# Optimization experiments

Measured on AMD Instinct MI355X. Metric: run time of the kernel, lower is better.

## Reference

```python
import jax, jax.numpy as jnp
import numpy as np

IN_FEATURES = 4096
OUT_FEATURES = 768
N_BITS = 8
BATCH = 4096


def setup_inputs() -> dict:
    key = jax.random.key(0)
    k1, k2, k3 = jax.random.split(key, 3)
    latent = jax.random.uniform(k1, (BATCH, IN_FEATURES), dtype=jnp.float32)
    true_sum = jax.random.uniform(k2, (BATCH, OUT_FEATURES * N_BITS), dtype=jnp.float32)
    # kaiming-normal-ish init: std = sqrt(2 / fan_in)
    weight = jax.random.normal(k3, (IN_FEATURES, OUT_FEATURES * N_BITS), dtype=jnp.float32) * np.sqrt(2.0 / IN_FEATURES)
    return {"latent": latent, "true_sum": true_sum, "weight": weight, "n_bits": N_BITS}


def reference(latent, true_sum, weight, n_bits):
    in_features = weight.shape[0]
    batch = latent.shape[0]
    # powers of two, MSB negated (two's-complement style decode)
    powers = (2.0 ** jnp.arange(n_bits, dtype=jnp.float32))
    powers = powers.at[-1].multiply(-1.0)

    prob_weights = jax.nn.sigmoid(weight)                      # [in, out*n_bits]
    # decode soft bits -> integer-valued weights: [in, out]
    int_weights = (prob_weights.reshape(in_features, -1, n_bits) * powers).sum(-1)
    # decode target bits -> integer-valued sums: [batch, out]
    int_sum = (true_sum.reshape(batch, -1, n_bits) * powers).sum(-1)

    # (latent.unsqueeze(-1) * int_weights).sum(-2) is exactly a GEMM
    pred = latent @ int_weights                                # [batch, out]

    scale_factor = 2.0 ** (n_bits - 1)
    recon_loss = jnp.mean((pred - int_sum) ** 2) / scale_factor
    polarize_loss = jnp.mean(prob_weights * (1.0 - prob_weights))
    return (recon_loss, polarize_loss)
```

## Files before the change

kernel.cpp:

```cpp
#include <hip/hip_runtime.h>
#include <stdint.h>

#define IN_F   4096
#define OUT_F  768
#define NB     8
#define BATCH  4096
#define WCOLS  (OUT_F*NB)

typedef short  bf16x8  __attribute__((ext_vector_type(8)));
typedef float  f32x4   __attribute__((ext_vector_type(4)));
typedef unsigned short ushort8 __attribute__((ext_vector_type(8)));

__device__ __forceinline__ unsigned short f2bf(float f){
    union { float f; uint32_t u; } v; v.f = f;
    uint32_t u = v.u;
    u += 0x7FFFu + ((u >> 16) & 1u);
    return (unsigned short)(u >> 16);
}

__device__ __forceinline__ void gload16(const void* g, void* l){
    __builtin_amdgcn_global_load_lds(
        (const __attribute__((address_space(1))) unsigned int*)g,
        (__attribute__((address_space(3))) unsigned int*)l, 16, 0, 0);
}

__global__ void prep_latent(const float* __restrict__ lat,
                            unsigned short* __restrict__ abf,
                            float* __restrict__ acc){
    if (blockIdx.x == 0 && threadIdx.x < 4) acc[threadIdx.x] = 0.f;
    int idx = (blockIdx.x * 256 + threadIdx.x) * 8;
    const float4* p = (const float4*)(lat + idx);
    float4 a = p[0], b = p[1];
    ushort8 o;
    o[0]=f2bf(a.x); o[1]=f2bf(a.y); o[2]=f2bf(a.z); o[3]=f2bf(a.w);
    o[4]=f2bf(b.x); o[5]=f2bf(b.y); o[6]=f2bf(b.z); o[7]=f2bf(b.w);
    *(ushort8*)(abf + idx) = o;
}

__global__ void decode_weight(const float* __restrict__ w,
                              unsigned short* __restrict__ bt,
                              float* __restrict__ acc){
    __shared__ unsigned short tile[64][70];
    __shared__ float part[4];
    const int tid = threadIdx.x;
    const int k0 = blockIdx.x * 64;
    const int n0 = blockIdx.y * 64;
    const int j     = tid & 63;
    const int ibase = (tid >> 6) * 16;
    float pol = 0.f;
    #pragma unroll 4
    for (int r = 0; r < 16; ++r){
        int i = ibase + r;
        const float4* src = (const float4*)(w + (size_t)(k0+i)*WCOLS + (size_t)(n0+j)*8);
        float4 a = src[0], b = src[1];
        float x[8] = {a.x,a.y,a.z,a.w,b.x,b.y,b.z,b.w};
        float p[8];
        #pragma unroll
        for (int q = 0; q < 8; ++q){
            p[q] = 1.f / (1.f + __expf(-x[q]));
            pol += p[q] * (1.f - p[q]);
        }
        float iw = p[0] + 2.f*p[1] + 4.f*p[2] + 8.f*p[3]
                 + 16.f*p[4] + 32.f*p[5] + 64.f*p[6] - 128.f*p[7];
        tile[j][i] = f2bf(iw);
    }
    #pragma unroll
    for (int off = 32; off; off >>= 1) pol += __shfl_down(pol, off);
    if ((tid & 63) == 0) part[tid >> 6] = pol;
    __syncthreads();
    const int nrow = tid >> 4;
    const int kb   = (tid & 15) * 4;
    #pragma unroll
    for (int q = 0; q < 4; ++q){
        int n = nrow + q*16;
        uint2 v;
        v.x = *(const unsigned int*)&tile[n][kb];
        v.y = *(const unsigned int*)&tile[n][kb+2];
        *(uint2*)(bt + (size_t)(n0+n)*IN_F + k0 + kb) = v;
    }
    if (tid == 0) atomicAdd(&acc[1], part[0]+part[1]+part[2]+part[3]);
}

#define BM 128
#define BN 96
#define BK 64
#define NT (IN_F/BK)
#define ABYTES (BM*BK*2)
#define BBYTES (BN*BK*2)

__launch_bounds__(256)
__global__ void gemm_loss(const unsigned short* __restrict__ abf,
                          const unsigned short* __restrict__ bt,
                          const float* __restrict__ ts,
                          float* __restrict__ acc){
    __shared__ unsigned short As[2][BM*BK];
    __shared__ unsigned short Bs[2][BN*BK];
    __shared__ float part[4];
    const int tid = threadIdx.x;
    const int w   = tid >> 6;
    const int l   = tid & 63;
    const int s   = l & 15, g = l >> 4;
    const int wr  = w >> 1, wc = w & 1;
    const int m0  = blockIdx.x * BM;
    const int n0  = blockIdx.y * BN;

    f32x4 accv[4][3];
    #pragma unroll
    for (int m = 0; m < 4; ++m)
        #pragma unroll
        for (int n = 0; n < 3; ++n)
            accv[m][n] = (f32x4){0.f,0.f,0.f,0.f};

    const int c8  = tid & 7;
    const int r0  = tid >> 3;
    const int scw = ((c8 ^ (r0 & 7)) << 3);
    const unsigned short* aS = abf + (size_t)(m0 + r0) * IN_F + scw;
    const unsigned short* bS = bt  + (size_t)(n0 + r0) * IN_F + scw;
    char* AsB = (char*)As;
    char* BsB = (char*)Bs;

    #define STAGE(kt, b) do {                                              \
        const int _ko = (kt) * BK;                                         \
        char* _ad = AsB + (b)*ABYTES + tid*16;                             \
        char* _bd = BsB + (b)*BBYTES + tid*16;                             \
        _Pragma("unroll")                                                  \
        for (int _i = 0; _i < 4; ++_i)                                     \
            gload16(aS + (size_t)_i*32*IN_F + _ko, _ad + _i*4096);         \
        _Pragma("unroll")                                                  \
        for (int _i = 0; _i < 3; ++_i)                                     \
            gload16(bS + (size_t)_i*32*IN_F + _ko, _bd + _i*4096);         \
    } while (0)

    #define COMPUTE(b) do {                                                \
        char* _Ab = AsB + (b)*ABYTES;                                      \
        char* _Bb = BsB + (b)*BBYTES;                                      \
        _Pragma("unroll")                                                  \
        for (int _kk = 0; _kk < 2; ++_kk){                                 \
            bf16x8 _af[4], _bf[3];                                         \
            _Pragma("unroll")                                              \
            for (int _m = 0; _m < 4; ++_m){                                \
                int _r  = wr*64 + _m*16 + s;                               \
                int _ch = _r*8 + ((_kk*4 + g) ^ (_r & 7));                 \
                _af[_m] = *(const bf16x8*)(_Ab + _ch*16);                  \
            }                                                              \
            _Pragma("unroll")                                              \
            for (int _n = 0; _n < 3; ++_n){                                \
                int _r  = wc*48 + _n*16 + s;                               \
                int _ch = _r*8 + ((_kk*4 + g) ^ (_r & 7));                 \
                _bf[_n] = *(const bf16x8*)(_Bb + _ch*16);                  \
            }                                                              \
            _Pragma("unroll")                                              \
            for (int _m = 0; _m < 4; ++_m)                                 \
                _Pragma("unroll")                                          \
                for (int _n = 0; _n < 3; ++_n)                             \
                    accv[_m][_n] = __builtin_amdgcn_mfma_f32_16x16x32_bf16(\
                        _af[_m], _bf[_n], accv[_m][_n], 0, 0, 0);          \
        }                                                                  \
    } while (0)

    STAGE(0, 0);
    __syncthreads();
    int cur = 0;
    for (int kt = 0; kt < NT; ++kt){
        if (kt + 1 < NT) STAGE(kt + 1, cur ^ 1);
        COMPUTE(cur);
        __syncthreads();
        cur ^= 1;
    }

    float local = 0.f;
    #pragma unroll
    for (int m = 0; m < 4; ++m){
        int rbase = m0 + wr*64 + m*16 + g*4;
        #pragma unroll
        for (int n = 0; n < 3; ++n){
            int col = n0 + wc*48 + n*16 + s;
            const float* tsp = ts + (size_t)rbase*WCOLS + (size_t)col*8;
            #pragma unroll
            for (int jj = 0; jj < 4; ++jj){
                const float4* q = (const float4*)(tsp + (size_t)jj*WCOLS);
                float4 x = q[0], y = q[1];
                float isum = x.x + 2.f*x.y + 4.f*x.z + 8.f*x.w
                           + 16.f*y.x + 32.f*y.y + 64.f*y.z - 128.f*y.w;
                float d = accv[m][n][jj] - isum;
                local += d*d;
            }
        }
    }
    #pragma unroll
    for (int off = 32; off; off >>= 1) local += __shfl_down(local, off);
    if (l == 0) part[w] = local;
    __syncthreads();
    if (tid == 0){
        atomicAdd(&acc[0], part[0]+part[1]+part[2]+part[3]);
    }
}

__global__ void finalize(const float* __restrict__ acc, float* __restrict__ out){
    out[0] = acc[0] * (1.0f / ((float)BATCH * (float)OUT_F * 128.0f));
    out[1] = acc[1] * (1.0f / ((float)IN_F * (float)WCOLS));
}

extern "C" void kernel_launch(void* const* d_in, const int* in_sizes, int n_in,
                              void* d_out, int out_size, void* d_ws, size_t ws_size,
                              hipStream_t stream){
    const float* latent   = (const float*)d_in[0];
    const float* true_sum = (const float*)d_in[1];
    const float* weight   = (const float*)d_in[2];
    float* acc = (float*)d_ws;
    unsigned short* abf = (unsigned short*)((char*)d_ws + 1024);
    unsigned short* bt  = (unsigned short*)((char*)d_ws + 1024 + (size_t)BATCH*IN_F*2);
    float* out = (float*)d_out;

    prep_latent<<<(BATCH*IN_F)/(256*8), 256, 0, stream>>>(latent, abf, acc);
    decode_weight<<<dim3(IN_F/64, OUT_F/64), 256, 0, stream>>>(weight, bt, acc);
    gemm_loss<<<dim3(BATCH/BM, OUT_F/BN), 256, 0, stream>>>(abf, bt, true_sum, acc);
    finalize<<<1, 1, 0, stream>>>(acc, out);
}
```

Baseline: 125.1 us.

## Use 4-stage LDS pipeline with vmcnt waits and pre-decode true_sum

Replaces the double-buffered GEMM loop with a four-buffer pipeline. Loads run three tiles ahead, and explicit vmcnt waits plus a single barrier per iteration replace the post-compute syncthreads. A separate kernel decodes true_sum into bf16 integer sums, so the GEMM epilogue reads a compact array instead of eight floats per output. The extra LDS cuts occupancy, and the bf16 rounding of the target sums adds precision loss to the loss value.

```diff
diff --git a/kernel.cpp b/kernel.cpp
--- a/kernel.cpp
+++ b/kernel.cpp
@@ -18,11 +18,21 @@
     return (unsigned short)(u >> 16);
 }
 
+__device__ __forceinline__ float bf2f(unsigned short u){
+    union { uint32_t q; float f; } v; v.q = ((uint32_t)u) << 16;
+    return v.f;
+}
+
 __device__ __forceinline__ void gload16(const void* g, void* l){
     __builtin_amdgcn_global_load_lds(
         (const __attribute__((address_space(1))) unsigned int*)g,
         (__attribute__((address_space(3))) unsigned int*)l, 16, 0, 0);
 }
+
+#define WAITV(n) do {                                                   \
+    asm volatile("s_waitcnt vmcnt(" #n ")" ::: "memory");               \
+    __builtin_amdgcn_sched_barrier(0);                                  \
+} while (0)
 
 __global__ void prep_latent(const float* __restrict__ lat,
                             unsigned short* __restrict__ abf,
@@ -81,20 +91,34 @@
     if (tid == 0) atomicAdd(&acc[1], part[0]+part[1]+part[2]+part[3]);
 }
 
+__global__ void ts_decode(const float* __restrict__ ts,
+                          unsigned short* __restrict__ isum){
+    const int tid = threadIdx.x;
+    #pragma unroll
+    for (int k = 0; k < 6; ++k){
+        int e = blockIdx.x * 1536 + k * 256 + tid;
+        const float4* q = (const float4*)(ts + (size_t)e * 8);
+        float4 x = q[0], y = q[1];
+        float v = x.x + 2.f*x.y + 4.f*x.z + 8.f*x.w
+                + 16.f*y.x + 32.f*y.y + 64.f*y.z - 128.f*y.w;
+        isum[e] = f2bf(v);
+    }
+}
+
 #define BM 128
 #define BN 96
 #define BK 64
 #define NT (IN_F/BK)
 #define ABYTES (BM*BK*2)
 #define BBYTES (BN*BK*2)
+#define BUFB   (ABYTES+BBYTES)
 
 __launch_bounds__(256)
 __global__ void gemm_loss(const unsigned short* __restrict__ abf,
                           const unsigned short* __restrict__ bt,
-                          const float* __restrict__ ts,
+                          const unsigned short* __restrict__ isum,
                           float* __restrict__ acc){
-    __shared__ unsigned short As[2][BM*BK];
-    __shared__ unsigned short Bs[2][BN*BK];
+    __shared__ char smem[4*BUFB];
     __shared__ float part[4];
     const int tid = threadIdx.x;
     const int w   = tid >> 6;
@@ -116,13 +140,11 @@
     const int scw = ((c8 ^ (r0 & 7)) << 3);
     const unsigned short* aS = abf + (size_t)(m0 + r0) * IN_F + scw;
     const unsigned short* bS = bt  + (size_t)(n0 + r0) * IN_F + scw;
-    char* AsB = (char*)As;
-    char* BsB = (char*)Bs;
-
-    #define STAGE(kt, b) do {                                              \
+
+    #define STAGE(kt, base) do {                                           \
         const int _ko = (kt) * BK;                                         \
-        char* _ad = AsB + (b)*ABYTES + tid*16;                             \
-        char* _bd = BsB + (b)*BBYTES + tid*16;                             \
+        char* _ad = (base) + tid*16;                                       \
+        char* _bd = (base) + ABYTES + tid*16;                              \
         _Pragma("unroll")                                                  \
         for (int _i = 0; _i < 4; ++_i)                                     \
             gload16(aS + (size_t)_i*32*IN_F + _ko, _ad + _i*4096);         \
@@ -131,9 +153,9 @@
             gload16(bS + (size_t)_i*32*IN_F + _ko, _bd + _i*4096);         \
     } while (0)
 
-    #define COMPUTE(b) do {                                                \
-        char* _Ab = AsB + (b)*ABYTES;                                      \
-        char* _Bb = BsB + (b)*BBYTES;                                      \
+    #define COMPUTE(base) do {                                             \
+        char* _Ab = (base);                                                \
+        char* _Bb = (base) + ABYTES;                                       \
         _Pragma("unroll")                                                  \
         for (int _kk = 0; _kk < 2; ++_kk){                                 \
             bf16x8 _af[4], _bf[3];                                         \
@@ -158,15 +180,24 @@
         }                                                                  \
     } while (0)
 
-    STAGE(0, 0);
-    __syncthreads();
-    int cur = 0;
-    for (int kt = 0; kt < NT; ++kt){
-        if (kt + 1 < NT) STAGE(kt + 1, cur ^ 1);
-        COMPUTE(cur);
-        __syncthreads();
-        cur ^= 1;
-    }
+    char* b0 = smem;
+    char* b1 = smem + BUFB;
+    char* b2 = smem + 2*BUFB;
+    char* b3 = smem + 3*BUFB;
+
+    STAGE(0, b0);
+    STAGE(1, b1);
+    STAGE(2, b2);
+    for (int t = 0; t < NT-3; ++t){
+        WAITV(14);
+        __builtin_amdgcn_s_barrier();
+        STAGE(t+3, b3);
+        COMPUTE(b0);
+        char* tmp = b0; b0 = b1; b1 = b2; b2 = b3; b3 = tmp;
+    }
+    WAITV(14); __builtin_amdgcn_s_barrier(); COMPUTE(b0);
+    WAITV(7);  __builtin_amdgcn_s_barrier(); COMPUTE(b1);
+    WAITV(0);  __builtin_amdgcn_s_barrier(); COMPUTE(b2);
 
     float local = 0.f;
     #pragma unroll
@@ -175,14 +206,10 @@
         #pragma unroll
         for (int n = 0; n < 3; ++n){
             int col = n0 + wc*48 + n*16 + s;
-            const float* tsp = ts + (size_t)rbase*WCOLS + (size_t)col*8;
             #pragma unroll
             for (int jj = 0; jj < 4; ++jj){
-                const float4* q = (const float4*)(tsp + (size_t)jj*WCOLS);
-                float4 x = q[0], y = q[1];
-                float isum = x.x + 2.f*x.y + 4.f*x.z + 8.f*x.w
-                           + 16.f*y.x + 32.f*y.y + 64.f*y.z - 128.f*y.w;
-                float d = accv[m][n][jj] - isum;
+                float is = bf2f(isum[(size_t)(rbase+jj)*OUT_F + col]);
+                float d = accv[m][n][jj] - is;
                 local += d*d;
             }
         }
@@ -208,12 +235,15 @@
     const float* true_sum = (const float*)d_in[1];
     const float* weight   = (const float*)d_in[2];
     float* acc = (float*)d_ws;
-    unsigned short* abf = (unsigned short*)((char*)d_ws + 1024);
-    unsigned short* bt  = (unsigned short*)((char*)d_ws + 1024 + (size_t)BATCH*IN_F*2);
+    unsigned short* abf  = (unsigned short*)((char*)d_ws + 1024);
+    unsigned short* bt   = (unsigned short*)((char*)d_ws + 1024 + (size_t)BATCH*IN_F*2);
+    unsigned short* isum = (unsigned short*)((char*)d_ws + 1024 + (size_t)BATCH*IN_F*2
+                                             + (size_t)OUT_F*IN_F*2);
     float* out = (float*)d_out;
 
     prep_latent<<<(BATCH*IN_F)/(256*8), 256, 0, stream>>>(latent, abf, acc);
     decode_weight<<<dim3(IN_F/64, OUT_F/64), 256, 0, stream>>>(weight, bt, acc);
-    gemm_loss<<<dim3(BATCH/BM, OUT_F/BN), 256, 0, stream>>>(abf, bt, true_sum, acc);
+    ts_decode<<<(BATCH*OUT_F)/(256*6), 256, 0, stream>>>(true_sum, isum);
+    gemm_loss<<<dim3(BATCH/BM, OUT_F/BN), 256, 0, stream>>>(abf, bt, isum, acc);
     finalize<<<1, 1, 0, stream>>>(acc, out);
 }
```

Measured after the change: 133.1 us. 6.4% more time.

## Split-K GEMM into two halves, move loss to separate pass, merge decode kernels

Applied to the files above, without the earlier changes.

The GEMM now uses a split-K of two. It launches 512 blocks instead of 256 so more CUs on the device are occupied, and each block writes its partial prediction slab to workspace. A new loss_pass kernel sums the two slabs, decodes true_sum and reduces the squared error into per-block partials. The latent and weight decode kernels are merged into one launch, and atomics are replaced by deterministic partial buffers that a 256-thread finalize kernel reduces. MFMA sections get s_setprio, in exchange for extra traffic writing and re-reading about 25MB of fp32 prediction slabs.

```diff
diff --git a/kernel.cpp b/kernel.cpp
--- a/kernel.cpp
+++ b/kernel.cpp
@@ -6,6 +6,7 @@
 #define NB     8
 #define BATCH  4096
 #define WCOLS  (OUT_F*NB)
+#define PREDN  (BATCH*OUT_F)
 
 typedef short  bf16x8  __attribute__((ext_vector_type(8)));
 typedef float  f32x4   __attribute__((ext_vector_type(4)));
@@ -24,85 +25,88 @@
         (__attribute__((address_space(3))) unsigned int*)l, 16, 0, 0);
 }
 
-__global__ void prep_latent(const float* __restrict__ lat,
-                            unsigned short* __restrict__ abf,
-                            float* __restrict__ acc){
-    if (blockIdx.x == 0 && threadIdx.x < 4) acc[threadIdx.x] = 0.f;
-    int idx = (blockIdx.x * 256 + threadIdx.x) * 8;
-    const float4* p = (const float4*)(lat + idx);
-    float4 a = p[0], b = p[1];
-    ushort8 o;
-    o[0]=f2bf(a.x); o[1]=f2bf(a.y); o[2]=f2bf(a.z); o[3]=f2bf(a.w);
-    o[4]=f2bf(b.x); o[5]=f2bf(b.y); o[6]=f2bf(b.z); o[7]=f2bf(b.w);
-    *(ushort8*)(abf + idx) = o;
-}
-
-__global__ void decode_weight(const float* __restrict__ w,
-                              unsigned short* __restrict__ bt,
-                              float* __restrict__ acc){
+__launch_bounds__(256)
+__global__ void decode_all(const float* __restrict__ w,
+                           const float* __restrict__ lat,
+                           unsigned short* __restrict__ bt,
+                           unsigned short* __restrict__ abf,
+                           float* __restrict__ polp){
     __shared__ unsigned short tile[64][70];
     __shared__ float part[4];
     const int tid = threadIdx.x;
-    const int k0 = blockIdx.x * 64;
-    const int n0 = blockIdx.y * 64;
-    const int j     = tid & 63;
-    const int ibase = (tid >> 6) * 16;
-    float pol = 0.f;
-    #pragma unroll 4
-    for (int r = 0; r < 16; ++r){
-        int i = ibase + r;
-        const float4* src = (const float4*)(w + (size_t)(k0+i)*WCOLS + (size_t)(n0+j)*8);
-        float4 a = src[0], b = src[1];
-        float x[8] = {a.x,a.y,a.z,a.w,b.x,b.y,b.z,b.w};
-        float p[8];
-        #pragma unroll
-        for (int q = 0; q < 8; ++q){
-            p[q] = 1.f / (1.f + __expf(-x[q]));
-            pol += p[q] * (1.f - p[q]);
+    const int bid = blockIdx.x;
+    if (bid < 768){
+        const int k0 = (bid & 63) * 64;
+        const int n0 = (bid >> 6) * 64;
+        const int j     = tid & 63;
+        const int ibase = (tid >> 6) * 16;
+        float pol = 0.f;
+        #pragma unroll 4
+        for (int r = 0; r < 16; ++r){
+            int i = ibase + r;
+            const float4* src = (const float4*)(w + (size_t)(k0+i)*WCOLS + (size_t)(n0+j)*8);
+            float4 a = src[0], b = src[1];
+            float x[8] = {a.x,a.y,a.z,a.w,b.x,b.y,b.z,b.w};
+            float p[8];
+            #pragma unroll
+            for (int q = 0; q < 8; ++q){
+                p[q] = 1.f / (1.f + __expf(-x[q]));
+                pol += p[q] * (1.f - p[q]);
+            }
+            float iw = p[0] + 2.f*p[1] + 4.f*p[2] + 8.f*p[3]
+                     + 16.f*p[4] + 32.f*p[5] + 64.f*p[6] - 128.f*p[7];
+            tile[j][i] = f2bf(iw);
         }
-        float iw = p[0] + 2.f*p[1] + 4.f*p[2] + 8.f*p[3]
-                 + 16.f*p[4] + 32.f*p[5] + 64.f*p[6] - 128.f*p[7];
-        tile[j][i] = f2bf(iw);
-    }
-    #pragma unroll
-    for (int off = 32; off; off >>= 1) pol += __shfl_down(pol, off);
-    if ((tid & 63) == 0) part[tid >> 6] = pol;
-    __syncthreads();
-    const int nrow = tid >> 4;
-    const int kb   = (tid & 15) * 4;
-    #pragma unroll
-    for (int q = 0; q < 4; ++q){
-        int n = nrow + q*16;
-        uint2 v;
-        v.x = *(const unsigned int*)&tile[n][kb];
-        v.y = *(const unsigned int*)&tile[n][kb+2];
-        *(uint2*)(bt + (size_t)(n0+n)*IN_F + k0 + kb) = v;
-    }
-    if (tid == 0) atomicAdd(&acc[1], part[0]+part[1]+part[2]+part[3]);
+        #pragma unroll
+        for (int off = 32; off; off >>= 1) pol += __shfl_down(pol, off);
+        if ((tid & 63) == 0) part[tid >> 6] = pol;
+        __syncthreads();
+        const int nrow = tid >> 4;
+        const int kb   = (tid & 15) * 4;
+        #pragma unroll
+        for (int q = 0; q < 4; ++q){
+            int n = nrow + q*16;
+            uint2 v;
+            v.x = *(const unsigned int*)&tile[n][kb];
+            v.y = *(const unsigned int*)&tile[n][kb+2];
+            *(uint2*)(bt + (size_t)(n0+n)*IN_F + k0 + kb) = v;
+        }
+        if (tid == 0) polp[bid] = part[0]+part[1]+part[2]+part[3];
+    } else {
+        int idx = ((bid - 768) * 256 + tid) * 8;
+        const float4* p = (const float4*)(lat + idx);
+        float4 a = p[0], b = p[1];
+        ushort8 o;
+        o[0]=f2bf(a.x); o[1]=f2bf(a.y); o[2]=f2bf(a.z); o[3]=f2bf(a.w);
+        o[4]=f2bf(b.x); o[5]=f2bf(b.y); o[6]=f2bf(b.z); o[7]=f2bf(b.w);
+        *(ushort8*)(abf + idx) = o;
+    }
 }
 
 #define BM 128
 #define BN 96
 #define BK 64
-#define NT (IN_F/BK)
+#define NTH 32
 #define ABYTES (BM*BK*2)
 #define BBYTES (BN*BK*2)
-
-__launch_bounds__(256)
-__global__ void gemm_loss(const unsigned short* __restrict__ abf,
+#define BUFB   (ABYTES+BBYTES)
+
+__launch_bounds__(256)
+__global__ void gemm_pred(const unsigned short* __restrict__ abf,
                           const unsigned short* __restrict__ bt,
-                          const float* __restrict__ ts,
-                          float* __restrict__ acc){
-    __shared__ unsigned short As[2][BM*BK];
-    __shared__ unsigned short Bs[2][BN*BK];
-    __shared__ float part[4];
+                          float* __restrict__ pred){
+    __shared__ __align__(16) char smem[2*BUFB];
     const int tid = threadIdx.x;
     const int w   = tid >> 6;
     const int l   = tid & 63;
     const int s   = l & 15, g = l >> 4;
     const int wr  = w >> 1, wc = w & 1;
-    const int m0  = blockIdx.x * BM;
-    const int n0  = blockIdx.y * BN;
+    const int bid  = blockIdx.x;
+    const int half = bid >> 8;
+    const int rem  = bid & 255;
+    const int m0   = (rem >> 3) * BM;
+    const int n0   = (rem & 7)  * BN;
+    const int kb   = half * (NTH*BK);
 
     f32x4 accv[4][3];
     #pragma unroll
@@ -114,15 +118,13 @@
     const int c8  = tid & 7;
     const int r0  = tid >> 3;
     const int scw = ((c8 ^ (r0 & 7)) << 3);
-    const unsigned short* aS = abf + (size_t)(m0 + r0) * IN_F + scw;
-    const unsigned short* bS = bt  + (size_t)(n0 + r0) * IN_F + scw;
-    char* AsB = (char*)As;
-    char* BsB = (char*)Bs;
-
-    #define STAGE(kt, b) do {                                              \
+    const unsigned short* aS = abf + (size_t)(m0 + r0) * IN_F + kb + scw;
+    const unsigned short* bS = bt  + (size_t)(n0 + r0) * IN_F + kb + scw;
+
+    #define STAGE(kt, base) do {                                           \
         const int _ko = (kt) * BK;                                         \
-        char* _ad = AsB + (b)*ABYTES + tid*16;                             \
-        char* _bd = BsB + (b)*BBYTES + tid*16;                             \
+        char* _ad = (base) + tid*16;                                       \
+        char* _bd = (base) + ABYTES + tid*16;                              \
         _Pragma("unroll")                                                  \
         for (int _i = 0; _i < 4; ++_i)                                     \
             gload16(aS + (size_t)_i*32*IN_F + _ko, _ad + _i*4096);         \
@@ -131,9 +133,9 @@
             gload16(bS + (size_t)_i*32*IN_F + _ko, _bd + _i*4096);         \
     } while (0)
 
-    #define COMPUTE(b) do {                                                \
-        char* _Ab = AsB + (b)*ABYTES;                                      \
-        char* _Bb = BsB + (b)*BBYTES;                                      \
+    #define COMPUTE(base) do {                                             \
+        char* _Ab = (base);                                                \
+        char* _Bb = (base) + ABYTES;                                       \
         _Pragma("unroll")                                                  \
         for (int _kk = 0; _kk < 2; ++_kk){                                 \
             bf16x8 _af[4], _bf[3];                                         \
@@ -149,56 +151,89 @@
                 int _ch = _r*8 + ((_kk*4 + g) ^ (_r & 7));                 \
                 _bf[_n] = *(const bf16x8*)(_Bb + _ch*16);                  \
             }                                                              \
+            __builtin_amdgcn_s_setprio(1);                                 \
             _Pragma("unroll")                                              \
             for (int _m = 0; _m < 4; ++_m)                                 \
                 _Pragma("unroll")                                          \
                 for (int _n = 0; _n < 3; ++_n)                             \
                     accv[_m][_n] = __builtin_amdgcn_mfma_f32_16x16x32_bf16(\
                         _af[_m], _bf[_n], accv[_m][_n], 0, 0, 0);          \
+            __builtin_amdgcn_s_setprio(0);                                 \
         }                                                                  \
     } while (0)
 
-    STAGE(0, 0);
+    char* b0 = smem;
+    char* b1 = smem + BUFB;
+    STAGE(0, b0);
     __syncthreads();
-    int cur = 0;
-    for (int kt = 0; kt < NT; ++kt){
-        if (kt + 1 < NT) STAGE(kt + 1, cur ^ 1);
-        COMPUTE(cur);
+    for (int t = 0; t < NTH; ++t){
+        if (t + 1 < NTH) STAGE(t + 1, (t & 1) ? b0 : b1);
+        COMPUTE((t & 1) ? b1 : b0);
         __syncthreads();
-        cur ^= 1;
-    }
-
-    float local = 0.f;
+    }
+
+    float* slab = pred + (size_t)half * PREDN;
     #pragma unroll
     for (int m = 0; m < 4; ++m){
         int rbase = m0 + wr*64 + m*16 + g*4;
         #pragma unroll
         for (int n = 0; n < 3; ++n){
             int col = n0 + wc*48 + n*16 + s;
-            const float* tsp = ts + (size_t)rbase*WCOLS + (size_t)col*8;
             #pragma unroll
-            for (int jj = 0; jj < 4; ++jj){
-                const float4* q = (const float4*)(tsp + (size_t)jj*WCOLS);
-                float4 x = q[0], y = q[1];
-                float isum = x.x + 2.f*x.y + 4.f*x.z + 8.f*x.w
-                           + 16.f*y.x + 32.f*y.y + 64.f*y.z - 128.f*y.w;
-                float d = accv[m][n][jj] - isum;
-                local += d*d;
-            }
+            for (int jj = 0; jj < 4; ++jj)
+                slab[(size_t)(rbase+jj)*OUT_F + col] = accv[m][n][jj];
         }
     }
+}
+
+__launch_bounds__(256)
+__global__ void loss_pass(const float* __restrict__ pred,
+                          const float* __restrict__ ts,
+                          float* __restrict__ lossp){
+    __shared__ float part[4];
+    const int tid = threadIdx.x;
+    const int e0  = (blockIdx.x * 256 + tid) * 2;
+    float local = 0.f;
+    #pragma unroll
+    for (int q = 0; q < 2; ++q){
+        int e = e0 + q;
+        float p = pred[e] + pred[(size_t)PREDN + e];
+        const float4* r = (const float4*)(ts + (size_t)e * 8);
+        float4 x = r[0], y = r[1];
+        float is = x.x + 2.f*x.y + 4.f*x.z + 8.f*x.w
+                 + 16.f*y.x + 32.f*y.y + 64.f*y.z - 128.f*y.w;
+        float d = p - is;
+        local += d*d;
+    }
     #pragma unroll
     for (int off = 32; off; off >>= 1) local += __shfl_down(local, off);
-    if (l == 0) part[w] = local;
+    if ((tid & 63) == 0) part[tid >> 6] = local;
+    __syncthreads();
+    if (tid == 0) lossp[blockIdx.x] = part[0]+part[1]+part[2]+part[3];
+}
+
+__launch_bounds__(256)
+__global__ void finalize(const float* __restrict__ lossp,
+                         const float* __restrict__ polp,
+                         float* __restrict__ out){
+    __shared__ float sm[2][4];
+    const int tid = threadIdx.x;
+    float a = 0.f, b = 0.f;
+    for (int i = tid; i < 6144; i += 256) a += lossp[i];
+    for (int i = tid; i < 768;  i += 256) b += polp[i];
+    #pragma unroll
+    for (int off = 32; off; off >>= 1){
+        a += __shfl_down(a, off);
+        b += __shfl_down(b, off);
+    }
+    if ((tid & 63) == 0){ sm[0][tid >> 6] = a; sm[1][tid >> 6] = b; }
     __syncthreads();
     if (tid == 0){
-        atomicAdd(&acc[0], part[0]+part[1]+part[2]+part[3]);
-    }
-}
-
-__global__ void finalize(const float* __restrict__ acc, float* __restrict__ out){
-    out[0] = acc[0] * (1.0f / ((float)BATCH * (float)OUT_F * 128.0f));
-    out[1] = acc[1] * (1.0f / ((float)IN_F * (float)WCOLS));
+        float sa = sm[0][0]+sm[0][1]+sm[0][2]+sm[0][3];
+        float sb = sm[1][0]+sm[1][1]+sm[1][2]+sm[1][3];
+        out[0] = sa * (1.0f / ((float)BATCH * (float)OUT_F * 128.0f));
+        out[1] = sb * (1.0f / ((float)IN_F * (float)WCOLS));
+    }
 }
 
 extern "C" void kernel_launch(void* const* d_in, const int* in_sizes, int n_in,
@@ -207,13 +242,16 @@
     const float* latent   = (const float*)d_in[0];
     const float* true_sum = (const float*)d_in[1];
     const float* weight   = (const float*)d_in[2];
-    float* acc = (float*)d_ws;
-    unsigned short* abf = (unsigned short*)((char*)d_ws + 1024);
-    unsigned short* bt  = (unsigned short*)((char*)d_ws + 1024 + (size_t)BATCH*IN_F*2);
+    char* ws = (char*)d_ws;
+    float* lossp = (float*)ws;
+    float* polp  = (float*)(ws + 32768);
+    unsigned short* bt  = (unsigned short*)(ws + 65536);
+    unsigned short* abf = (unsigned short*)(ws + 65536 + 6291456);
+    float* pred = (float*)(ws + 65536 + 6291456 + 33554432);
     float* out = (float*)d_out;
 
-    prep_latent<<<(BATCH*IN_F)/(256*8), 256, 0, stream>>>(latent, abf, acc);
-    decode_weight<<<dim3(IN_F/64, OUT_F/64), 256, 0, stream>>>(weight, bt, acc);
-    gemm_loss<<<dim3(BATCH/BM, OUT_F/BN), 256, 0, stream>>>(abf, bt, true_sum, acc);
-    finalize<<<1, 1, 0, stream>>>(acc, out);
-}
+    decode_all<<<768 + 8192, 256, 0, stream>>>(weight, latent, bt, abf, polp);
+    gemm_pred<<<512, 256, 0, stream>>>(abf, bt, pred);
+    loss_pass<<<PREDN/512, 256, 0, stream>>>(pred, true_sum, lossp);
+    finalize<<<1, 256, 0, stream>>>(lossp, polp, out);
+}
```

Measured after the change: 109.8 us. 1.14x faster.
